# Optimization experiments

Measured on AMD Instinct MI355X. Metric: run time of the kernel, lower is better.

Reference implementation:

```python
import jax, jax.numpy as jnp
import numpy as np

N = 50000
E = 640000
IN_DIM = 128
HIDDEN = 128
OUT_DIM = 128


def setup_inputs() -> dict:
    key = jax.random.key(0)
    ks = jax.random.split(key, 8)
    x = jax.random.normal(ks[0], (N, IN_DIM), dtype=jnp.float32)
    edge_index = jax.random.randint(ks[1], (2, E), 0, N, dtype=jnp.int64)
    s = 1.0 / np.sqrt(IN_DIM)
    w1l = jax.random.uniform(ks[2], (HIDDEN, IN_DIM), minval=-s, maxval=s, dtype=jnp.float32)
    b1 = jax.random.uniform(ks[3], (HIDDEN,), minval=-s, maxval=s, dtype=jnp.float32)
    w1r = jax.random.uniform(ks[4], (HIDDEN, IN_DIM), minval=-s, maxval=s, dtype=jnp.float32)
    s2 = 1.0 / np.sqrt(HIDDEN)
    w2l = jax.random.uniform(ks[5], (OUT_DIM, HIDDEN), minval=-s2, maxval=s2, dtype=jnp.float32)
    b2 = jax.random.uniform(ks[6], (OUT_DIM,), minval=-s2, maxval=s2, dtype=jnp.float32)
    w2r = jax.random.uniform(ks[7], (OUT_DIM, HIDDEN), minval=-s2, maxval=s2, dtype=jnp.float32)
    return {"x": x, "edge_index": edge_index, "w1l": w1l, "b1": b1, "w1r": w1r,
            "w2l": w2l, "b2": b2, "w2r": w2r}


def sage_conv(x, src, dst, wl, bl, wr):
    # mean-aggregate source features at destination nodes
    msg = x[src]                                   # [E, d]
    agg = jax.ops.segment_sum(msg, dst, num_segments=N)   # [N, d]
    cnt = jax.ops.segment_sum(jnp.ones((src.shape[0],), x.dtype), dst, num_segments=N)
    agg = agg / jnp.maximum(cnt, 1.0)[:, None]
    # PyG SAGEConv: lin_l(agg) + lin_r(x); bias lives in lin_l
    return agg @ wl.T + bl + x @ wr.T


def reference(x, edge_index, w1l, b1, w1r, w2l, b2, w2r):
    src, dst = edge_index[0], edge_index[1]
    h = jax.nn.relu(sage_conv(x, src, dst, w1l, b1, w1r))
    out = sage_conv(h, src, dst, w2l, b2, w2r)
    return out
```

## Files before the change

### kernel.cpp

```cpp
#include <hip/hip_runtime.h>

#define DIM 128
#define CAP 64
#define FSTRIDE 16

typedef _Float16 half8 __attribute__((ext_vector_type(8)));
typedef float floatx4 __attribute__((ext_vector_type(4)));
typedef unsigned short ushort8 __attribute__((ext_vector_type(8)));

__global__ void k_setup(const floatx4* __restrict__ in4, half8* __restrict__ out8,
                        const float* __restrict__ w1l, const float* __restrict__ w1r,
                        half8* __restrict__ Wf1,
                        const float* __restrict__ w2l, const float* __restrict__ w2r,
                        half8* __restrict__ Wf2,
                        const int* __restrict__ src, const int* __restrict__ dst,
                        int* __restrict__ fillS, unsigned short* __restrict__ pad,
                        int n8, int E, int bBucket){
  int b = blockIdx.x;
  if (b < bBucket){
    int e = b*256 + threadIdx.x;
    if (e < E){
      int d = dst[e];
      int p = atomicAdd(&fillS[d*FSTRIDE], 1);
      if (p < CAP) pad[d*CAP + p] = (unsigned short)src[e];
    }
  } else if (b < bBucket + ((n8 + 255) >> 8)){
    int i = (b - bBucket)*256 + threadIdx.x;
    if (i < n8){
      floatx4 a = in4[2*i], c = in4[2*i + 1];
      half8 h;
      h[0] = (_Float16)a[0]; h[1] = (_Float16)a[1];
      h[2] = (_Float16)a[2]; h[3] = (_Float16)a[3];
      h[4] = (_Float16)c[0]; h[5] = (_Float16)c[1];
      h[6] = (_Float16)c[2]; h[7] = (_Float16)c[3];
      out8[i] = h;
    }
  } else {
    int which = b - bBucket - ((n8 + 255) >> 8);
    const float* wl = (which < 16) ? w1l : w2l;
    const float* wr = (which < 16) ? w1r : w2r;
    half8* Wf = (which < 16) ? Wf1 : Wf2;
    int t = (which & 15)*256 + threadIdx.x;
    int ks = t >> 9, jt = (t >> 6) & 7, lane = t & 63;
    int j = jt*16 + (lane & 15);
    int kb = ks*32 + (lane >> 4)*8;
    half8 h;
    #pragma unroll
    for (int i = 0; i < 8; ++i){
      int k = kb + i;
      float v = (k < 128) ? wl[j*128 + k] : wr[j*128 + (k - 128)];
      h[i] = (_Float16)v;
    }
    Wf[t] = h;
  }
}

__global__ __launch_bounds__(256) void k_agg(
    const half8* __restrict__ featH8, const unsigned short* __restrict__ pad,
    const int* __restrict__ fillS, half8* __restrict__ aggH8, int n)
{
  int node = blockIdx.x*16 + (threadIdx.x >> 4);
  int ch = threadIdx.x & 15;
  if (node >= n) return;
  int deg = fillS[node*FSTRIDE];
  int cnt = (deg < CAP) ? deg : CAP;
  const int base = node*CAP;
  float acc[8] = {0,0,0,0,0,0,0,0};
  for (int p = 0; p < cnt; p += 8){
    ushort8 si = *(const ushort8*)&pad[base + p];
    int   s[8];
    float w[8];
    #pragma unroll
    for (int u = 0; u < 8; ++u){
      bool valid = (p + u) < cnt;
      s[u] = valid ? (int)si[u] : 0;
      w[u] = valid ? 1.0f : 0.0f;
    }
    half8 v[8];
    #pragma unroll
    for (int u = 0; u < 8; ++u) v[u] = featH8[s[u]*16 + ch];
    #pragma unroll
    for (int u = 0; u < 8; ++u){
      #pragma unroll
      for (int i = 0; i < 8; ++i) acc[i] += w[u] * (float)v[u][i];
    }
  }
  float sc = 1.0f / fmaxf((float)deg, 1.0f);
  half8 o;
  #pragma unroll
  for (int i = 0; i < 8; ++i) o[i] = (_Float16)(acc[i]*sc);
  aggH8[node*16 + ch] = o;
}

template<bool RELU, bool OUT_HALF>
__global__ __launch_bounds__(256) void k_gemm(
    const half8* __restrict__ aggH8, const half8* __restrict__ selfH8,
    const half8* __restrict__ Wf, const float* __restrict__ bias,
    void* __restrict__ outp, int n)
{
  const int tid = threadIdx.x;
  const int lane = tid & 63, wv = tid >> 6;
  const int m = lane & 15, quad = lane >> 4;
  const int node0 = blockIdx.x * 64;
  const int arow = node0 + wv*16 + m;
  const int rowSafe = (arow < n) ? arow : 0;

  floatx4 acc[8] = {{0,0,0,0},{0,0,0,0},{0,0,0,0},{0,0,0,0},
                    {0,0,0,0},{0,0,0,0},{0,0,0,0},{0,0,0,0}};

  #pragma unroll
  for (int ks = 0; ks < 8; ++ks){
    half8 a = (ks < 4) ? aggH8 [rowSafe*16 + (ks    *4 + quad)]
                       : selfH8[rowSafe*16 + ((ks-4)*4 + quad)];
    if (arow >= n) a = half8{};
    #pragma unroll
    for (int jt = 0; jt < 8; ++jt){
      half8 b = Wf[(ks*8 + jt)*64 + lane];
      acc[jt] = __builtin_amdgcn_mfma_f32_16x16x32_f16(a, b, acc[jt], 0, 0, 0);
    }
  }

  #pragma unroll
  for (int jt = 0; jt < 8; ++jt){
    int j = jt*16 + m;
    float bj = bias[j];
    #pragma unroll
    for (int r = 0; r < 4; ++r){
      int node = node0 + wv*16 + quad*4 + r;
      if (node < n){
        float v = acc[jt][r] + bj;
        if (RELU) v = fmaxf(v, 0.f);
        if (OUT_HALF) ((_Float16*)outp)[node*DIM + j] = (_Float16)v;
        else          ((float*)outp)[node*DIM + j] = v;
      }
    }
  }
}

extern "C" void kernel_launch(void* const* d_in, const int* in_sizes, int n_in,
                              void* d_out, int out_size, void* d_ws, size_t ws_size,
                              hipStream_t stream)
{
  const float* x   = (const float*)d_in[0];
  const int*   ei  = (const int*)d_in[1];
  const float* w1l = (const float*)d_in[2];
  const float* b1  = (const float*)d_in[3];
  const float* w1r = (const float*)d_in[4];
  const float* w2l = (const float*)d_in[5];
  const float* b2  = (const float*)d_in[6];
  const float* w2r = (const float*)d_in[7];
  float* out = (float*)d_out;

  const int N = in_sizes[0] / DIM;
  const int E = in_sizes[1] / 2;

  char* p = (char*)d_ws;
  auto carve = [&](size_t bytes) -> char* {
    char* q = p;
    p += (bytes + 255) & ~(size_t)255;
    return q;
  };
  _Float16*       xh    = (_Float16*)carve((size_t)N * DIM * 2);
  _Float16*       hh    = (_Float16*)carve((size_t)N * DIM * 2);
  _Float16*       aggH  = (_Float16*)carve((size_t)N * DIM * 2);
  half8*          Wf1   = (half8*)carve(4096 * 16);
  half8*          Wf2   = (half8*)carve(4096 * 16);
  int*            fillS = (int*)carve((size_t)N * FSTRIDE * 4);
  unsigned short* pad   = (unsigned short*)carve((size_t)N * CAP * 2);

  const int* src = ei;
  const int* dst = ei + E;

  const int n8 = N * DIM / 8;
  const int bCast = (n8 + 255)/256;
  const int bBucket = (E + 255)/256;

  hipMemsetAsync(fillS, 0, (size_t)N * FSTRIDE * 4, stream);

  k_setup<<<bBucket + bCast + 32, 256, 0, stream>>>(
      (const floatx4*)x, (half8*)xh, w1l, w1r, Wf1, w2l, w2r, Wf2,
      src, dst, fillS, pad, n8, E, bBucket);

  const int gAgg = (N + 15)/16;
  const int gGemm = (N + 63)/64;

  k_agg<<<gAgg, 256, 0, stream>>>((const half8*)xh, pad, fillS, (half8*)aggH, N);
  k_gemm<true, true><<<gGemm, 256, 0, stream>>>(
      (const half8*)aggH, (const half8*)xh, Wf1, b1, (void*)hh, N);
  k_agg<<<gAgg, 256, 0, stream>>>((const half8*)hh, pad, fillS, (half8*)aggH, N);
  k_gemm<false, false><<<gGemm, 256, 0, stream>>>(
      (const half8*)aggH, (const half8*)hh, Wf2, b2, (void*)out, N);
}
```

Before: 204.7 us.

## Partition edge bucketing by destination range across block groups

Replaces one-thread-per-edge bucketing with 8 destination-node partitions times 320 edge chunks. Each block scans its edge chunk and inserts only edges whose destination falls in its partition, so atomics and pad writes for a partition stay in a narrow address range. The intent is better atomic and cache locality, likely helped by consecutive block IDs covering different partitions of the same chunk, which may then run on different XCDs. The cost is that every edge's dst is read 8 times, and fill order changes so which edges land in pad beyond CAP can differ.

```diff
diff --git a/kernel.cpp b/kernel.cpp
--- a/kernel.cpp
+++ b/kernel.cpp
@@ -3,6 +3,7 @@
 #define DIM 128
 #define CAP 64
 #define FSTRIDE 16
+#define PBLK 320
 
 typedef _Float16 half8 __attribute__((ext_vector_type(8)));
 typedef float floatx4 __attribute__((ext_vector_type(4)));
@@ -15,17 +16,26 @@
                         half8* __restrict__ Wf2,
                         const int* __restrict__ src, const int* __restrict__ dst,
                         int* __restrict__ fillS, unsigned short* __restrict__ pad,
-                        int n8, int E, int bBucket){
+                        int n8, int N, int E){
   int b = blockIdx.x;
-  if (b < bBucket){
-    int e = b*256 + threadIdx.x;
-    if (e < E){
+  if (b < 8*PBLK){
+    const int p = b & 7, c = b >> 3;
+    const int PN = (N + 7) >> 3;
+    const int n0 = p * PN;
+    const int n1 = (n0 + PN < N) ? n0 + PN : N;
+    const int CE = (E + PBLK - 1) / PBLK;
+    const int e0 = c * CE;
+    const int e1 = (e0 + CE < E) ? e0 + CE : E;
+    for (int e = e0 + threadIdx.x; e < e1; e += 256){
       int d = dst[e];
-      int p = atomicAdd(&fillS[d*FSTRIDE], 1);
-      if (p < CAP) pad[d*CAP + p] = (unsigned short)src[e];
-    }
-  } else if (b < bBucket + ((n8 + 255) >> 8)){
-    int i = (b - bBucket)*256 + threadIdx.x;
+      if (d >= n0 && d < n1){
+        int s = src[e];
+        int q = atomicAdd(&fillS[d*FSTRIDE], 1);
+        if (q < CAP) pad[d*CAP + q] = (unsigned short)s;
+      }
+    }
+  } else if (b < 8*PBLK + ((n8 + 255) >> 8)){
+    int i = (b - 8*PBLK)*256 + threadIdx.x;
     if (i < n8){
       floatx4 a = in4[2*i], c = in4[2*i + 1];
       half8 h;
@@ -36,7 +46,7 @@
       out8[i] = h;
     }
   } else {
-    int which = b - bBucket - ((n8 + 255) >> 8);
+    int which = b - 8*PBLK - ((n8 + 255) >> 8);
     const float* wl = (which < 16) ? w1l : w2l;
     const float* wr = (which < 16) ? w1r : w2r;
     half8* Wf = (which < 16) ? Wf1 : Wf2;
@@ -173,13 +183,12 @@
 
   const int n8 = N * DIM / 8;
   const int bCast = (n8 + 255)/256;
-  const int bBucket = (E + 255)/256;
 
   hipMemsetAsync(fillS, 0, (size_t)N * FSTRIDE * 4, stream);
 
-  k_setup<<<bBucket + bCast + 32, 256, 0, stream>>>(
+  k_setup<<<8*PBLK + bCast + 32, 256, 0, stream>>>(
       (const floatx4*)x, (half8*)xh, w1l, w1r, Wf1, w2l, w2r, Wf2,
-      src, dst, fillS, pad, n8, E, bBucket);
+      src, dst, fillS, pad, n8, N, E);
 
   const int gAgg = (N + 15)/16;
   const int gGemm = (N + 63)/64;
```

New measurement: 203.4 us. About the same (-0.7%).
